# Performance work log

Measured on AMD Instinct MI355X. Metric: run time of the kernel, lower is better.

The kernel has to match this reference:

```python
import jax, jax.numpy as jnp
import numpy as np

B, CIN, COUT, K, L = 32, 128, 128, 7, 4096
STRIDE, PAD = 1, 3
TEMP = 1.0


def setup_inputs() -> dict:
    key = jax.random.key(0)
    k1, k2 = jax.random.split(key)
    x = jax.random.normal(k1, (B, CIN, L), dtype=jnp.float32)
    weight = jax.random.normal(k2, (COUT, CIN, K), dtype=jnp.float32) * 0.1  # init: normal(0, 0.1)
    bias = jnp.zeros((COUT,), dtype=jnp.float32)
    return {"x": x, "weight": weight, "bias": bias}


def reference(x, weight, bias):
    # Soft tropical conv (intended math of the module):
    #   y[b,o,w] = T * logsumexp_{c,k}( (x[b,c,w*stride+k] + W[o,c,k]) / T ) + bias[o]
    # with -inf padding (exp(-inf)=0 => plain zero padding in exp space).
    # Computed as a numerically-stabilized standard conv in exp space, which is
    # mathematically identical and avoids materializing the (B,O,C,K,L) tensor.
    xm = jnp.max(x)
    wm = jnp.max(weight)
    ex = jnp.exp((x - xm) / TEMP)          # (B, CIN, L)
    ew = jnp.exp((weight - wm) / TEMP)     # (COUT, CIN, K)
    s = jax.lax.conv_general_dilated(
        ex, ew,
        window_strides=(STRIDE,),
        padding=[(PAD, PAD)],
        dimension_numbers=("NCH", "OIH", "NCH"),
    )  # (B, COUT, L_out); cross-correlation, matching torch unfold indexing x[i+k]
    y = TEMP * jnp.log(s) + (xm + wm)
    return y + bias[None, :, None]
```

## Files before the change

### kernel.cpp

```cpp
#include <hip/hip_runtime.h>
#include <hip/hip_bf16.h>
#include <cstdint>
#include <cstddef>

#define B_N   32
#define CIN_  128
#define COUT_ 128
#define KW_   7
#define L_    4096
#define PAD_  3
#define NW_   128
#define BC_   32
#define RPB   4104
#define NWELEM (KW_ * COUT_ * CIN_)
#define NGUARD (B_N * 8 * CIN_)

#define SW_ELEMS (KW_ * COUT_ * BC_)
#define SX_ROWS  192
#define SX_ELEMS (SX_ROWS * BC_)
#define NGRAN_W  (SW_ELEMS / 8)
#define NGRAN_T  ((SW_ELEMS + SX_ELEMS) / 8)

typedef __attribute__((ext_vector_type(8))) short  bf16x8;
typedef __attribute__((ext_vector_type(4))) float  f32x4;

__device__ __forceinline__ void gl2lds16(const void* g, void* l) {
    __builtin_amdgcn_global_load_lds(
        (const __attribute__((address_space(1))) unsigned int*)g,
        (__attribute__((address_space(3))) unsigned int*)l, 16, 0, 0);
}

__global__ void prep_wg_kernel(const float* __restrict__ w,
                               __hip_bfloat16* __restrict__ ewb,
                               __hip_bfloat16* __restrict__ exT) {
    int idx = blockIdx.x * 256 + threadIdx.x;
    if (idx < NWELEM) {
        int c = idx & 127, rest = idx >> 7;
        int o = rest & 127, k = rest >> 7;
        ewb[idx] = __float2bfloat16(__expf(w[(o * CIN_ + c) * KW_ + k]));
    } else if (idx < NWELEM + NGUARD) {
        int j  = idx - NWELEM;
        int b  = j >> 10, rr = (j >> 7) & 7, c = j & 127;
        int r  = (rr < 3) ? rr : (4096 + rr);
        exT[((size_t)b * RPB + r) * CIN_ + c] = __float2bfloat16(0.0f);
    }
}

__global__ __launch_bounds__(256) void exp_x_kernel(
        const float* __restrict__ x, __hip_bfloat16* __restrict__ exT) {
    __shared__ __align__(16) __hip_bfloat16 tileT[64 * 136];
    const int b  = blockIdx.y;
    const int l0 = blockIdx.x * 64;
    const int tid = threadIdx.x;
    const float* xb = x + (size_t)b * CIN_ * L_ + l0;

    #pragma unroll
    for (int i = 0; i < 8; ++i) {
        int idx = tid + 256 * i;
        int c   = idx >> 4;
        int lv4 = (idx & 15) * 4;
        f32x4 v = *(const f32x4*)(xb + (size_t)c * L_ + lv4);
        #pragma unroll
        for (int k2 = 0; k2 < 4; ++k2) {
            int l  = lv4 + k2;
            int sw = (l >> 2) & 15;
            tileT[l * 136 + (c ^ (sw << 3))] = __float2bfloat16(__expf(v[k2]));
        }
    }
    __syncthreads();

    __hip_bfloat16* dst = exT + ((size_t)b * RPB + l0 + PAD_) * CIN_;
    #pragma unroll
    for (int i = 0; i < 4; ++i) {
        int idx = tid + 256 * i;
        int l  = idx >> 4;
        int gc = idx & 15;
        int sw = (l >> 2) & 15;
        bf16x8 vv = *(const bf16x8*)&tileT[l * 136 + ((gc ^ sw) << 3)];
        *(bf16x8*)(dst + (size_t)l * CIN_ + gc * 8) = vv;
    }
}

__global__ __launch_bounds__(256, 2) void tropconv_kernel(
        const __hip_bfloat16* __restrict__ exT,
        const __hip_bfloat16* __restrict__ ewb,
        const float* __restrict__ bias,
        float* __restrict__ out) {
    __shared__ __align__(16) __hip_bfloat16 smem[SW_ELEMS + SX_ELEMS];
    __hip_bfloat16* sW = smem;
    __hip_bfloat16* sX = smem + SW_ELEMS;

    const int tid  = threadIdx.x;
    const int lane = tid & 63;
    const int wave = tid >> 6;
    const int wm   = wave >> 1;
    const int wn   = wave & 1;
    const int l15  = lane & 15;
    const int q    = lane >> 4;

    const int b  = blockIdx.y;
    const int w0 = blockIdx.x * NW_;
    const __hip_bfloat16* exb = exT + ((size_t)b * RPB + w0) * CIN_;

    f32x4 acc[4][4];
    #pragma unroll
    for (int i = 0; i < 4; ++i)
        #pragma unroll
        for (int j = 0; j < 4; ++j)
            acc[i][j] = (f32x4){0.f, 0.f, 0.f, 0.f};

    for (int c = 0; c < 4; ++c) {
        const int c0 = c * BC_;

        #pragma unroll
        for (int s = 0; s < 17; ++s) {
            int g = tid + 256 * s;
            if (g < NGRAN_W) {
                int row = g >> 2, j = g & 3;
                gl2lds16(ewb + ((size_t)row << 7) + c0 + j * 8, &sW[g * 8]);
            } else {
                int gx = g - NGRAN_W;
                int p = gx >> 2, j = gx & 3;
                gl2lds16(exb + ((size_t)p << 7) + c0 + j * 8, &sX[gx * 8]);
            }
        }
        __syncthreads();

        #pragma unroll
        for (int t = 0; t < KW_; ++t) {
            bf16x8 af[4], bx[4];
            #pragma unroll
            for (int mi = 0; mi < 4; ++mi) {
                int o = wm * 64 + mi * 16 + l15;
                af[mi] = *(const bf16x8*)&sW[(t * COUT_ + o) * BC_ + q * 8];
            }
            #pragma unroll
            for (int ni = 0; ni < 4; ++ni) {
                int p = wn * 64 + ni * 16 + l15 + t;
                bx[ni] = *(const bf16x8*)&sX[p * BC_ + q * 8];
            }
            #pragma unroll
            for (int mi = 0; mi < 4; ++mi)
                #pragma unroll
                for (int ni = 0; ni < 4; ++ni)
                    acc[mi][ni] = __builtin_amdgcn_mfma_f32_16x16x32_bf16(
                        af[mi], bx[ni], acc[mi][ni], 0, 0, 0);
        }
        __syncthreads();
    }

    float* outb = out + (size_t)b * COUT_ * L_;
    #pragma unroll
    for (int mi = 0; mi < 4; ++mi) {
        #pragma unroll
        for (int r = 0; r < 4; ++r) {
            int o = wm * 64 + mi * 16 + q * 4 + r;
            float bv = bias[o];
            #pragma unroll
            for (int ni = 0; ni < 4; ++ni) {
                int w = w0 + wn * 64 + ni * 16 + l15;
                outb[(size_t)o * L_ + w] = __logf(acc[mi][ni][r]) + bv;
            }
        }
    }
}

extern "C" void kernel_launch(void* const* d_in, const int* in_sizes, int n_in,
                              void* d_out, int out_size, void* d_ws, size_t ws_size,
                              hipStream_t stream) {
    const float* x    = (const float*)d_in[0];
    const float* wgt  = (const float*)d_in[1];
    const float* bias = (const float*)d_in[2];
    float* out = (float*)d_out;

    __hip_bfloat16* exT = (__hip_bfloat16*)d_ws;
    __hip_bfloat16* ewb = (__hip_bfloat16*)((char*)d_ws + (size_t)B_N * RPB * CIN_ * 2);

    prep_wg_kernel<<<(NWELEM + NGUARD + 255) / 256, 256, 0, stream>>>(wgt, ewb, exT);
    exp_x_kernel<<<dim3(L_ / 64, B_N), 256, 0, stream>>>(x, exT);
    tropconv_kernel<<<dim3(L_ / NW_, B_N), 256, 0, stream>>>(exT, ewb, bias, out);
}
```

Baseline: 147.5 us.

## Double conv tile width, swizzle LDS chunks, rotate channel order across blocks

Widens each block's output tile from 128 to 256 positions, so every wave computes 4x8 MFMA tiles and the weight tile loaded into LDS is reused across twice as many outputs. It also XOR-swizzles the 16-byte chunks in LDS to cut bank conflicts on fragment reads, and rotates the starting channel chunk for half the blocks to spread memory traffic. In exchange the accumulators double, which raises register pressure and may lower occupancy, and the grid is halved to 512 blocks.

```diff
diff --git a/kernel.cpp b/kernel.cpp
--- a/kernel.cpp
+++ b/kernel.cpp
@@ -9,17 +9,17 @@
 #define KW_   7
 #define L_    4096
 #define PAD_  3
-#define NW_   128
+#define NW_   256
 #define BC_   32
 #define RPB   4104
 #define NWELEM (KW_ * COUT_ * CIN_)
 #define NGUARD (B_N * 8 * CIN_)
 
+#define SXROWS   264
 #define SW_ELEMS (KW_ * COUT_ * BC_)
-#define SX_ROWS  192
-#define SX_ELEMS (SX_ROWS * BC_)
+#define SX_ELEMS (SXROWS * BC_)
 #define NGRAN_W  (SW_ELEMS / 8)
-#define NGRAN_T  ((SW_ELEMS + SX_ELEMS) / 8)
+#define NGRAN_X  (SX_ELEMS / 8)
 
 typedef __attribute__((ext_vector_type(8))) short  bf16x8;
 typedef __attribute__((ext_vector_type(4))) float  f32x4;
@@ -101,48 +101,56 @@
     const int b  = blockIdx.y;
     const int w0 = blockIdx.x * NW_;
     const __hip_bfloat16* exb = exT + ((size_t)b * RPB + w0) * CIN_;
+    const int rot = ((blockIdx.x + (blockIdx.y << 4)) >> 8) & 1;
 
-    f32x4 acc[4][4];
+    f32x4 acc[4][8];
     #pragma unroll
     for (int i = 0; i < 4; ++i)
         #pragma unroll
-        for (int j = 0; j < 4; ++j)
+        for (int j = 0; j < 8; ++j)
             acc[i][j] = (f32x4){0.f, 0.f, 0.f, 0.f};
 
-    for (int c = 0; c < 4; ++c) {
-        const int c0 = c * BC_;
+    for (int ci = 0; ci < 4; ++ci) {
+        const int c0 = ((ci + rot * 2) & 3) * BC_;
 
         #pragma unroll
-        for (int s = 0; s < 17; ++s) {
+        for (int s = 0; s < 18; ++s) {
             int g = tid + 256 * s;
             if (g < NGRAN_W) {
-                int row = g >> 2, j = g & 3;
+                int row = g >> 2, j = (g & 3) ^ (row & 3);
                 gl2lds16(ewb + ((size_t)row << 7) + c0 + j * 8, &sW[g * 8]);
             } else {
                 int gx = g - NGRAN_W;
-                int p = gx >> 2, j = gx & 3;
-                gl2lds16(exb + ((size_t)p << 7) + c0 + j * 8, &sX[gx * 8]);
+                int row = gx >> 2, j = (gx & 3) ^ (row & 3);
+                gl2lds16(exb + ((size_t)row << 7) + c0 + j * 8, &sX[gx * 8]);
             }
+        }
+        if (tid < 32) {
+            int gx = tid + (18 * 256 - NGRAN_W);
+            int row = gx >> 2, j = (gx & 3) ^ (row & 3);
+            gl2lds16(exb + ((size_t)row << 7) + c0 + j * 8, &sX[gx * 8]);
         }
         __syncthreads();
 
         #pragma unroll
         for (int t = 0; t < KW_; ++t) {
-            bf16x8 af[4], bx[4];
+            bf16x8 af[4], bx[8];
             #pragma unroll
             for (int mi = 0; mi < 4; ++mi) {
-                int o = wm * 64 + mi * 16 + l15;
-                af[mi] = *(const bf16x8*)&sW[(t * COUT_ + o) * BC_ + q * 8];
+                int row = t * COUT_ + wm * 64 + mi * 16 + l15;
+                int slot = q ^ (row & 3);
+                af[mi] = *(const bf16x8*)&sW[row * BC_ + slot * 8];
             }
             #pragma unroll
-            for (int ni = 0; ni < 4; ++ni) {
-                int p = wn * 64 + ni * 16 + l15 + t;
-                bx[ni] = *(const bf16x8*)&sX[p * BC_ + q * 8];
+            for (int ni = 0; ni < 8; ++ni) {
+                int row = wn * 128 + ni * 16 + l15 + t;
+                int slot = q ^ (row & 3);
+                bx[ni] = *(const bf16x8*)&sX[row * BC_ + slot * 8];
             }
             #pragma unroll
             for (int mi = 0; mi < 4; ++mi)
                 #pragma unroll
-                for (int ni = 0; ni < 4; ++ni)
+                for (int ni = 0; ni < 8; ++ni)
                     acc[mi][ni] = __builtin_amdgcn_mfma_f32_16x16x32_bf16(
                         af[mi], bx[ni], acc[mi][ni], 0, 0, 0);
         }
@@ -157,8 +165,8 @@
             int o = wm * 64 + mi * 16 + q * 4 + r;
             float bv = bias[o];
             #pragma unroll
-            for (int ni = 0; ni < 4; ++ni) {
-                int w = w0 + wn * 64 + ni * 16 + l15;
+            for (int ni = 0; ni < 8; ++ni) {
+                int w = w0 + wn * 128 + ni * 16 + l15;
                 outb[(size_t)o * L_ + w] = __logf(acc[mi][ni][r]) + bv;
             }
         }
```

Result: slower. 183.4 us (+24.4%).
